# Optimization experiments

Hardware: AMD Instinct MI355X
Metric: run time of the kernel (lower is better)

Reference implementation:

```python
import jax, jax.numpy as jnp
import numpy as np

VOCAB, DIM, HEADS, LAYERS = 32000, 1024, 16, 2
B, S = 2, 1024
HD = DIM // HEADS


def rmsnorm(x, g, eps=1e-6):
    return x * jax.lax.rsqrt(jnp.mean(x * x, axis=-1, keepdims=True) + eps) * g


def setup_inputs() -> dict:
    key = jax.random.key(0)
    ks = jax.random.split(key, 20)
    s = 0.02
    d = {
        "text_ids": jax.random.randint(ks[0], (B, S), 0, VOCAB),
        "embed": jax.random.normal(ks[1], (VOCAB, DIM), jnp.float32) * s,
        "g1": jnp.ones((LAYERS, DIM), jnp.float32),
        "wq": jax.random.normal(ks[2], (LAYERS, DIM, DIM), jnp.float32) * s,
        "bq": jnp.zeros((LAYERS, DIM), jnp.float32),
        "wk": jax.random.normal(ks[3], (LAYERS, DIM, DIM), jnp.float32) * s,
        "bk": jnp.zeros((LAYERS, DIM), jnp.float32),
        "wv": jax.random.normal(ks[4], (LAYERS, DIM, DIM), jnp.float32) * s,
        "bv": jnp.zeros((LAYERS, DIM), jnp.float32),
        "wo": jax.random.normal(ks[5], (LAYERS, DIM, DIM), jnp.float32) * s,
        "bo": jnp.zeros((LAYERS, DIM), jnp.float32),
        "g2": jnp.ones((LAYERS, DIM), jnp.float32),
        "w1": jax.random.normal(ks[6], (LAYERS, DIM, 4 * DIM), jnp.float32) * s,
        "b1": jnp.zeros((LAYERS, 4 * DIM), jnp.float32),
        "w2": jax.random.normal(ks[7], (LAYERS, 4 * DIM, DIM), jnp.float32) * s,
        "b2": jnp.zeros((LAYERS, DIM), jnp.float32),
        "gf": jnp.ones((DIM,), jnp.float32),
        "head_w": jax.random.normal(ks[8], (DIM, VOCAB), jnp.float32) * s,
        "head_b": jnp.zeros((VOCAB,), jnp.float32),
    }
    return d


def reference(text_ids, embed, g1, wq, bq, wk, bk, wv, bv, wo, bo,
              g2, w1, b1, w2, b2, gf, head_w, head_b):
    b, s = text_ids.shape
    x = embed[text_ids]                                   # [B,S,D]
    causal = jnp.tril(jnp.ones((s, s), dtype=bool))        # [S,S]
    scale = 1.0 / jnp.sqrt(jnp.asarray(HD, x.dtype))
    for l in range(LAYERS):
        # attention sublayer: x = x + attn(norm1(x))
        h = rmsnorm(x, g1[l])
        q = (h @ wq[l] + bq[l]).reshape(b, s, HEADS, HD)
        k = (h @ wk[l] + bk[l]).reshape(b, s, HEADS, HD)
        v = (h @ wv[l] + bv[l]).reshape(b, s, HEADS, HD)
        scores = jnp.einsum("bqhd,bkhd->bhqk", q, k) * scale
        scores = jnp.where(causal, scores, jnp.asarray(-1e30, scores.dtype))
        a = jax.nn.softmax(scores, axis=-1)
        o = jnp.einsum("bhqk,bkhd->bqhd", a, v).reshape(b, s, DIM)
        x = x + (o @ wo[l] + bo[l])
        # FFN sublayer: x = x + ffn(norm2(x)), SiLU MLP (MoE unused in source forward)
        h2 = rmsnorm(x, g2[l])
        x = x + (jax.nn.silu(h2 @ w1[l] + b1[l]) @ w2[l] + b2[l])
    x = rmsnorm(x, gf)
    return x.astype(jnp.float32) @ head_w + head_b         # [B,S,VOCAB]
```

## Files before the change

kernel.cpp:

```cpp
#include <hip/hip_runtime.h>

#define LAYERS 2
#define DIM 1024
#define HEADS 16
#define HD 64
#define BATCH 2
#define SEQ 1024
#define ROWS (BATCH * SEQ)
#define FFN (4 * DIM)
#define VOCAB 32000
#define QKVN (3 * DIM)

typedef unsigned short u16;
typedef short vshort8 __attribute__((ext_vector_type(8)));
typedef float f32x4 __attribute__((ext_vector_type(4)));

#define VMCNT(n) asm volatile("s_waitcnt vmcnt(" #n ")" ::: "memory")

__device__ __forceinline__ u16 f2bf(float f) {
  union { float f; unsigned u; } x{f};
  unsigned r = (x.u + 0x7fffu + ((x.u >> 16) & 1u)) >> 16;
  return (u16)r;
}

__device__ __forceinline__ void gll16(const void* g, u16* l) {
  __builtin_amdgcn_global_load_lds(
      (const __attribute__((address_space(1))) void*)g,
      (__attribute__((address_space(3))) void*)l, 16, 0, 0);
}

__device__ __forceinline__ int xcd_swizzle(int orig, int nwg) {
  int q = nwg >> 3, r = nwg & 7;
  int xcd = orig & 7;
  int base = (xcd < r) ? xcd * (q + 1) : r * (q + 1) + (xcd - r) * q;
  return base + (orig >> 3);
}

__global__ __launch_bounds__(256) void transpose_f32_bf16(
    const float* __restrict__ src, u16* __restrict__ dst, int R, int C) {
  __shared__ float tile[32][33];
  int c0 = blockIdx.x * 32, r0 = blockIdx.y * 32;
  int tx = threadIdx.x, ty = threadIdx.y;
#pragma unroll
  for (int i = 0; i < 4; i++)
    tile[ty + i * 8][tx] = src[(size_t)(r0 + ty + i * 8) * C + c0 + tx];
  __syncthreads();
#pragma unroll
  for (int i = 0; i < 4; i++)
    dst[(size_t)(c0 + ty + i * 8) * R + r0 + tx] = f2bf(tile[tx][ty + i * 8]);
}

__global__ __launch_bounds__(256) void pack_qkv_bias(
    const float* __restrict__ bq, const float* __restrict__ bk,
    const float* __restrict__ bv, float* __restrict__ o) {
  int t = blockIdx.x * 256 + threadIdx.x;
  if (t < DIM) o[t] = bq[t];
  else if (t < 2 * DIM) o[t] = bk[t - DIM];
  else if (t < 3 * DIM) o[t] = bv[t - 2 * DIM];
}

__global__ __launch_bounds__(256) void embed_gather(
    const int* __restrict__ ids, const float* __restrict__ emb,
    float* __restrict__ x) {
  int row = blockIdx.x;
  int id = ids[row];
  const float4* s = (const float4*)(emb + (size_t)id * DIM);
  float4* d = (float4*)(x + (size_t)row * DIM);
  d[threadIdx.x] = s[threadIdx.x];
}

__global__ __launch_bounds__(256) void rmsnorm_kernel(
    const float* __restrict__ x, const float* __restrict__ g,
    u16* __restrict__ out) {
  int row = blockIdx.x;
  int t = threadIdx.x;
  const float4* xr = (const float4*)(x + (size_t)row * DIM);
  float4 v = xr[t];
  float ss = v.x * v.x + v.y * v.y + v.z * v.z + v.w * v.w;
  for (int off = 32; off > 0; off >>= 1) ss += __shfl_down(ss, off);
  __shared__ float part[4];
  if ((t & 63) == 0) part[t >> 6] = ss;
  __syncthreads();
  float tot = part[0] + part[1] + part[2] + part[3];
  float r = rsqrtf(tot / (float)DIM + 1e-6f);
  float4 gv = ((const float4*)g)[t];
  ushort4 o;
  o.x = f2bf(v.x * r * gv.x);
  o.y = f2bf(v.y * r * gv.y);
  o.z = f2bf(v.z * r * gv.z);
  o.w = f2bf(v.w * r * gv.w);
  *(ushort4*)(out + (size_t)row * DIM + t * 4) = o;
}

__global__ __launch_bounds__(256) void addnorm_kernel(
    float* __restrict__ x, const float* __restrict__ P0,
    const float* __restrict__ P1, const float* __restrict__ bias,
    const float* __restrict__ g, u16* __restrict__ h) {
  int row = blockIdx.x;
  int t = threadIdx.x;
  float4 v = ((const float4*)(x + (size_t)row * DIM))[t];
  float4 a = ((const float4*)(P0 + (size_t)row * DIM))[t];
  float4 b = ((const float4*)(P1 + (size_t)row * DIM))[t];
  float4 c = ((const float4*)bias)[t];
  v.x += a.x + b.x + c.x;
  v.y += a.y + b.y + c.y;
  v.z += a.z + b.z + c.z;
  v.w += a.w + b.w + c.w;
  ((float4*)(x + (size_t)row * DIM))[t] = v;
  float ss = v.x * v.x + v.y * v.y + v.z * v.z + v.w * v.w;
  for (int off = 32; off > 0; off >>= 1) ss += __shfl_down(ss, off);
  __shared__ float part[4];
  if ((t & 63) == 0) part[t >> 6] = ss;
  __syncthreads();
  float tot = part[0] + part[1] + part[2] + part[3];
  float r = rsqrtf(tot / (float)DIM + 1e-6f);
  float4 gv = ((const float4*)g)[t];
  ushort4 o;
  o.x = f2bf(v.x * r * gv.x);
  o.y = f2bf(v.y * r * gv.y);
  o.z = f2bf(v.z * r * gv.z);
  o.w = f2bf(v.w * r * gv.w);
  *(ushort4*)(h + (size_t)row * DIM + t * 4) = o;
}

template <int OUTBF, int SILU, int SPLITK, int MFAST>
__global__ __launch_bounds__(256, 2) void gemm128_kernel(
    const u16* __restrict__ A, const u16* __restrict__ Wt,
    const float* __restrict__ bias, void* __restrict__ outv,
    float* __restrict__ pout1, int M, int N, int K) {
  __shared__ u16 As[2][128 * 64];
  __shared__ u16 Bs[2][128 * 64];
  int nm = M >> 7, nn = N >> 7, nwg = nm * nn;
  int wg = xcd_swizzle(blockIdx.x, SPLITK ? nwg * 2 : nwg);
  int ks = 0;
  if (SPLITK) { ks = wg >= nwg; wg -= ks * nwg; }
  int mi, ni;
  if (MFAST) { mi = wg % nm; ni = wg / nm; }
  else       { ni = wg % nn; mi = wg / nn; }
  int m0 = mi << 7, n0 = ni << 7;
  int kb = SPLITK ? ks * (K >> 1) : 0;
  int NTt = (SPLITK ? (K >> 1) : K) >> 6;
  int tid = threadIdx.x, wave = tid >> 6, lane = tid & 63;
  int wr = wave >> 1, wc = wave & 1;
  int r16 = lane & 15, g4 = lane >> 4;
  int lrow = lane >> 3, lslot = lane & 7;

  f32x4 acc[4][4] = {};

  auto stage = [&](int buf, int kt) {
#pragma unroll
    for (int i = 0; i < 4; i++) {
      int s = wave * 4 + i;
      int row = s * 8 + lrow;
      int slot = lslot ^ (row & 7);
      gll16(A + (size_t)(m0 + row) * K + kb + kt * 64 + slot * 8,
            &As[buf][s * 512 + lane * 8]);
    }
#pragma unroll
    for (int i = 0; i < 4; i++) {
      int s = wave * 4 + i;
      int row = s * 8 + lrow;
      int slot = lslot ^ (row & 7);
      gll16(Wt + (size_t)(n0 + row) * K + kb + kt * 64 + slot * 8,
            &Bs[buf][s * 512 + lane * 8]);
    }
  };

  stage(0, 0);
  VMCNT(0);
  __builtin_amdgcn_s_barrier();

  for (int t = 0; t < NTt; t++) {
    int cur = t & 1;
    if (t + 1 < NTt) stage(cur ^ 1, t + 1);
#pragma unroll
    for (int kk = 0; kk < 2; kk++) {
      vshort8 af[4], bf[4];
#pragma unroll
      for (int m = 0; m < 4; m++) {
        int r = wr * 64 + m * 16 + r16;
        int slot = (kk * 4 + g4) ^ (r & 7);
        af[m] = *(const vshort8*)&As[cur][r * 64 + slot * 8];
      }
#pragma unroll
      for (int n = 0; n < 4; n++) {
        int c = wc * 64 + n * 16 + r16;
        int slot = (kk * 4 + g4) ^ (c & 7);
        bf[n] = *(const vshort8*)&Bs[cur][c * 64 + slot * 8];
      }
#pragma unroll
      for (int m = 0; m < 4; m++)
#pragma unroll
        for (int n = 0; n < 4; n++)
          acc[m][n] = __builtin_amdgcn_mfma_f32_16x16x32_bf16(af[m], bf[n],
                                                              acc[m][n], 0, 0, 0);
    }
    VMCNT(0);
    __builtin_amdgcn_s_barrier();
  }

  if (SPLITK) {
    float* P = ks ? pout1 : (float*)outv;
#pragma unroll
    for (int m = 0; m < 4; m++) {
      int rowb = m0 + wr * 64 + m * 16 + g4 * 4;
#pragma unroll
      for (int n = 0; n < 4; n++) {
        int col = n0 + wc * 64 + n * 16 + r16;
#pragma unroll
        for (int j = 0; j < 4; j++)
          P[(size_t)(rowb + j) * N + col] = acc[m][n][j];
      }
    }
  } else {
#pragma unroll
    for (int m = 0; m < 4; m++) {
      int rowb = m0 + wr * 64 + m * 16 + g4 * 4;
#pragma unroll
      for (int n = 0; n < 4; n++) {
        int col = n0 + wc * 64 + n * 16 + r16;
        float b = bias[col];
#pragma unroll
        for (int j = 0; j < 4; j++) {
          float v = acc[m][n][j] + b;
          if (SILU) v = v / (1.f + __expf(-v));
          if (OUTBF)
            ((u16*)outv)[(size_t)(rowb + j) * N + col] = f2bf(v);
          else
            ((float*)outv)[(size_t)(rowb + j) * N + col] = v;
        }
      }
    }
  }
}

__global__ __launch_bounds__(512, 2) void gemm256_kernel(
    const u16* __restrict__ A, const u16* __restrict__ Wt,
    const float* __restrict__ bias, float* __restrict__ out,
    int M, int N, int K) {
  __shared__ u16 As[2][256 * 64];
  __shared__ u16 Bs[2][256 * 64];
  int nm = M >> 8, nn = N >> 8;
  int wg = xcd_swizzle(blockIdx.x, nm * nn);
  int mi = wg % nm, ni = wg / nm;
  int m0 = mi << 8, n0 = ni << 8;
  int tid = threadIdx.x, w = tid >> 6, lane = tid & 63;
  int wr = w >> 2, wc = w & 3;
  int r16 = lane & 15, g4 = lane >> 4;
  int srow8 = lane >> 3, sslot = lane & 7;
  int NT = K >> 6;

  f32x4 acc[8][4] = {};

  auto stageA = [&](int buf, int t, int hb, int j) {
    int chunk = j * 8 + w;
    int row = hb * 128 + chunk * 8 + srow8;
    int slot = sslot ^ (row & 7);
    gll16(A + (size_t)(m0 + row) * K + t * 64 + slot * 8,
          &As[buf][hb * 8192 + chunk * 512 + lane * 8]);
  };
  auto stageB = [&](int buf, int t, int hb, int j) {
    int chunk = j * 8 + w;
    int row = hb * 128 + chunk * 8 + srow8;
    int slot = sslot ^ (row & 7);
    gll16(Wt + (size_t)(n0 + row) * K + t * 64 + slot * 8,
          &Bs[buf][hb * 8192 + chunk * 512 + lane * 8]);
  };
  auto readA = [&](int buf, int mf, int kk) -> vshort8 {
    int row = mf * 32 + wr * 16 + r16;
    int slot = (kk * 4 + g4) ^ (row & 7);
    return *(const vshort8*)&As[buf][row * 64 + slot * 8];
  };
  auto readB = [&](int buf, int nf, int kk) -> vshort8 {
    int row = nf * 64 + wc * 16 + r16;
    int slot = (kk * 4 + g4) ^ (row & 7);
    return *(const vshort8*)&Bs[buf][row * 64 + slot * 8];
  };

  stageA(0, 0, 0, 0); stageA(0, 0, 0, 1);
  stageB(0, 0, 0, 0); stageB(0, 0, 0, 1);
  stageB(0, 0, 1, 0); stageB(0, 0, 1, 1);
  stageA(0, 0, 1, 0); stageA(0, 0, 1, 1);
  VMCNT(0);
  __builtin_amdgcn_s_barrier();

  vshort8 af[4][2], bf0[2][2], bf1[2][2];

  for (int t = 0; t < NT; t++) {
    int cur = t & 1, nxt = cur ^ 1;
    bool hn = (t + 1 < NT);
#pragma unroll
    for (int m = 0; m < 4; m++)
#pragma unroll
      for (int kk = 0; kk < 2; kk++) af[m][kk] = readA(cur, m, kk);
#pragma unroll
    for (int n = 0; n < 2; n++)
#pragma unroll
      for (int kk = 0; kk < 2; kk++) bf0[n][kk] = readB(cur, n, kk);
    if (hn) { stageA(nxt, t + 1, 0, 0); stageA(nxt, t + 1, 0, 1); }
    __builtin_amdgcn_s_barrier();
    __builtin_amdgcn_s_setprio(1);
#pragma unroll
    for (int m = 0; m < 4; m++)
#pragma unroll
      for (int n = 0; n < 2; n++)
#pragma unroll
        for (int kk = 0; kk < 2; kk++)
          acc[m][n] = __builtin_amdgcn_mfma_f32_16x16x32_bf16(
              af[m][kk], bf0[n][kk], acc[m][n], 0, 0, 0);
    __builtin_amdgcn_s_setprio(0);
    VMCNT(4);
    __builtin_amdgcn_s_barrier();
#pragma unroll
    for (int n = 0; n < 2; n++)
#pragma unroll
      for (int kk = 0; kk < 2; kk++) bf1[n][kk] = readB(cur, 2 + n, kk);
    if (hn) { stageB(nxt, t + 1, 0, 0); stageB(nxt, t + 1, 0, 1); }
    __builtin_amdgcn_s_barrier();
    __builtin_amdgcn_s_setprio(1);
#pragma unroll
    for (int m = 0; m < 4; m++)
#pragma unroll
      for (int n = 0; n < 2; n++)
#pragma unroll
        for (int kk = 0; kk < 2; kk++)
          acc[m][n + 2] = __builtin_amdgcn_mfma_f32_16x16x32_bf16(
              af[m][kk], bf1[n][kk], acc[m][n + 2], 0, 0, 0);
    __builtin_amdgcn_s_setprio(0);
    VMCNT(4);
    __builtin_amdgcn_s_barrier();
#pragma unroll
    for (int m = 0; m < 4; m++)
#pragma unroll
      for (int kk = 0; kk < 2; kk++) af[m][kk] = readA(cur, 4 + m, kk);
    if (hn) { stageB(nxt, t + 1, 1, 0); stageB(nxt, t + 1, 1, 1); }
    __builtin_amdgcn_s_barrier();
    __builtin_amdgcn_s_setprio(1);
#pragma unroll
    for (int m = 0; m < 4; m++)
#pragma unroll
      for (int n = 0; n < 2; n++)
#pragma unroll
        for (int kk = 0; kk < 2; kk++)
          acc[m + 4][n + 2] = __builtin_amdgcn_mfma_f32_16x16x32_bf16(
              af[m][kk], bf1[n][kk], acc[m + 4][n + 2], 0, 0, 0);
    __builtin_amdgcn_s_setprio(0);
    VMCNT(4);
    __builtin_amdgcn_s_barrier();
#pragma unroll
    for (int n = 0; n < 2; n++)
#pragma unroll
      for (int kk = 0; kk < 2; kk++) bf0[n][kk] = readB(cur, n, kk);
    if (hn) { stageA(nxt, t + 1, 1, 0); stageA(nxt, t + 1, 1, 1); }
    __builtin_amdgcn_s_barrier();
    __builtin_amdgcn_s_setprio(1);
#pragma unroll
    for (int m = 0; m < 4; m++)
#pragma unroll
      for (int n = 0; n < 2; n++)
#pragma unroll
        for (int kk = 0; kk < 2; kk++)
          acc[m + 4][n] = __builtin_amdgcn_mfma_f32_16x16x32_bf16(
              af[m][kk], bf0[n][kk], acc[m + 4][n], 0, 0, 0);
    __builtin_amdgcn_s_setprio(0);
    VMCNT(4);
    __builtin_amdgcn_s_barrier();
  }

#pragma unroll
  for (int mf = 0; mf < 8; mf++) {
    int rowb = m0 + mf * 32 + wr * 16 + g4 * 4;
#pragma unroll
    for (int nf = 0; nf < 4; nf++) {
      int col = n0 + nf * 64 + wc * 16 + r16;
      float b = bias[col];
#pragma unroll
      for (int j = 0; j < 4; j++)
        out[(size_t)(rowb + j) * N + col] = acc[mf][nf][j] + b;
    }
  }
}

__global__ __launch_bounds__(256) void vtrans_kernel(const u16* __restrict__ qkv,
                                                     u16* __restrict__ vt2) {
  __shared__ u16 tl[64][80];
  int s0 = blockIdx.x * 64;
  int bh = blockIdx.y;
  int b = bh >> 4, h = bh & 15;
  int tid = threadIdx.x;
#pragma unroll
  for (int c = 0; c < 2; c++) {
    int idx = tid + c * 256;
    int row = idx >> 3;
    int col8 = (idx & 7) * 8;
    *(vshort8*)&tl[row][col8] = *(const vshort8*)
        &qkv[(size_t)(b * SEQ + s0 + row) * QKVN + 2 * DIM + h * HD + col8];
  }
  __syncthreads();
#pragma unroll
  for (int c = 0; c < 2; c++) {
    int idx = tid + c * 256;
    int s8l = idx >> 6;
    int d = idx & 63;
    vshort8 v;
#pragma unroll
    for (int j = 0; j < 8; j++) v[j] = (short)tl[s8l * 8 + j][d];
    *(vshort8*)&vt2[(((size_t)bh * (SEQ / 8) + (s0 >> 3) + s8l) * 64 + d) * 8] = v;
  }
}

__global__ __launch_bounds__(256) void attn_kernel(const u16* __restrict__ qkv,
                                                   const u16* __restrict__ vt2,
                                                   u16* __restrict__ o) {
  __shared__ u16 Ks[2][32 * 64];
  __shared__ u16 pl[4][16 * 40];
  int qblk = blockIdx.x, bh = blockIdx.y;
  int b = bh >> 4, h = bh & 15;
  int tid = threadIdx.x, w = tid >> 6, lane = tid & 63;
  int r16 = lane & 15, g4 = lane >> 4;
  int q0 = qblk * 64 + w * 16;

  const u16* qrow = qkv + ((size_t)(b * SEQ) + q0 + r16) * QKVN + h * HD;
  vshort8 aq0 = *(const vshort8*)(qrow + g4 * 8);
  vshort8 aq1 = *(const vshort8*)(qrow + 32 + g4 * 8);

  float mrun[4], lrun[4];
  f32x4 accO[4];
#pragma unroll
  for (int j = 0; j < 4; j++) { mrun[j] = -1e30f; lrun[j] = 0.f; }
#pragma unroll
  for (int d = 0; d < 4; d++) accO[d] = f32x4{0.f, 0.f, 0.f, 0.f};

  int nkvT = qblk * 2 + 2;
  auto stageK = [&](int buf, int kt) {
    int row = tid >> 3;
    int slot = (tid & 7) ^ (row & 7);
    gll16(qkv + ((size_t)(b * SEQ) + kt * 32 + row) * QKVN + DIM + h * HD + slot * 8,
          &Ks[buf][w * 512 + lane * 8]);
  };
  stageK(0, 0);
  __syncthreads();
  int buf = 0;
  for (int kt = 0; kt < nkvT; kt++) {
    int kv0 = kt * 32;
    if (kt + 1 < nkvT) stageK(buf ^ 1, kt + 1);
    if (kv0 <= q0 + 15) {
      int row0 = r16, row1 = 16 + r16;
      vshort8 bk00 = *(const vshort8*)&Ks[buf][row0 * 64 + ((0 + g4) ^ (row0 & 7)) * 8];
      vshort8 bk01 = *(const vshort8*)&Ks[buf][row0 * 64 + ((4 + g4) ^ (row0 & 7)) * 8];
      vshort8 bk10 = *(const vshort8*)&Ks[buf][row1 * 64 + ((0 + g4) ^ (row1 & 7)) * 8];
      vshort8 bk11 = *(const vshort8*)&Ks[buf][row1 * 64 + ((4 + g4) ^ (row1 & 7)) * 8];
      f32x4 s0 = {}, s1 = {};
      s0 = __builtin_amdgcn_mfma_f32_16x16x32_bf16(aq0, bk00, s0, 0, 0, 0);
      s0 = __builtin_amdgcn_mfma_f32_16x16x32_bf16(aq1, bk01, s0, 0, 0, 0);
      s1 = __builtin_amdgcn_mfma_f32_16x16x32_bf16(aq0, bk10, s1, 0, 0, 0);
      s1 = __builtin_amdgcn_mfma_f32_16x16x32_bf16(aq1, bk11, s1, 0, 0, 0);

#pragma unroll
      for (int j = 0; j < 4; j++) {
        int qg = q0 + g4 * 4 + j;
        float x0 = s0[j] * 0.125f;
        float x1 = s1[j] * 0.125f;
        if (kv0 + r16 > qg) x0 = -1e30f;
        if (kv0 + 16 + r16 > qg) x1 = -1e30f;
        float mx = fmaxf(x0, x1);
#pragma unroll
        for (int mm = 1; mm < 16; mm <<= 1) mx = fmaxf(mx, __shfl_xor(mx, mm));
        float mnew = fmaxf(mrun[j], mx);
        float alpha = __expf(mrun[j] - mnew);
        float p0 = __expf(x0 - mnew);
        float p1 = __expf(x1 - mnew);
        float rs = p0 + p1;
#pragma unroll
        for (int mm = 1; mm < 16; mm <<= 1) rs += __shfl_xor(rs, mm);
        lrun[j] = lrun[j] * alpha + rs;
        mrun[j] = mnew;
#pragma unroll
        for (int d = 0; d < 4; d++) accO[d][j] *= alpha;
        pl[w][(g4 * 4 + j) * 40 + r16] = f2bf(p0);
        pl[w][(g4 * 4 + j) * 40 + 16 + r16] = f2bf(p1);
      }
      asm volatile("s_waitcnt lgkmcnt(0)" ::: "memory");
      vshort8 ap = *(const vshort8*)&pl[w][r16 * 40 + g4 * 8];
      const u16* vbase = vt2 + (((size_t)bh * (SEQ / 8) + (kv0 >> 3) + g4) * 64) * 8;
#pragma unroll
      for (int d = 0; d < 4; d++) {
        vshort8 bv = *(const vshort8*)(vbase + (size_t)(d * 16 + r16) * 8);
        accO[d] = __builtin_amdgcn_mfma_f32_16x16x32_bf16(ap, bv, accO[d], 0, 0, 0);
      }
    }
    __syncthreads();
    buf ^= 1;
  }

#pragma unroll
  for (int j = 0; j < 4; j++) {
    float inv = 1.f / lrun[j];
    int row = q0 + g4 * 4 + j;
#pragma unroll
    for (int d = 0; d < 4; d++)
      o[((size_t)(b * SEQ) + row) * DIM + h * HD + d * 16 + r16] =
          f2bf(accO[d][j] * inv);
  }
}

extern "C" void kernel_launch(void* const* d_in, const int* in_sizes, int n_in,
                              void* d_out, int out_size, void* d_ws,
                              size_t ws_size, hipStream_t stream) {
  const int* ids = (const int*)d_in[0];
  const float* emb = (const float*)d_in[1];
  const float* g1 = (const float*)d_in[2];
  const float* wq = (const float*)d_in[3];
  const float* bq = (const float*)d_in[4];
  const float* wk = (const float*)d_in[5];
  const float* bk = (const float*)d_in[6];
  const float* wv = (const float*)d_in[7];
  const float* bv = (const float*)d_in[8];
  const float* wo = (const float*)d_in[9];
  const float* bo = (const float*)d_in[10];
  const float* g2 = (const float*)d_in[11];
  const float* w1 = (const float*)d_in[12];
  const float* b1 = (const float*)d_in[13];
  const float* w2 = (const float*)d_in[14];
  const float* b2 = (const float*)d_in[15];
  const float* gf = (const float*)d_in[16];
  const float* head_w = (const float*)d_in[17];
  const float* head_b = (const float*)d_in[18];
  float* out = (float*)d_out;

  char* ws = (char*)d_ws;
  size_t off = 0;
  auto alloc = [&](size_t bytes) -> char* {
    char* p = ws + off;
    off += (bytes + 255) & ~(size_t)255;
    return p;
  };
  u16* wqkvT = (u16*)alloc((size_t)LAYERS * QKVN * DIM * 2);
  u16* woT = (u16*)alloc((size_t)LAYERS * DIM * DIM * 2);
  u16* w1T = (u16*)alloc((size_t)LAYERS * DIM * FFN * 2);
  u16* w2T = (u16*)alloc((size_t)LAYERS * DIM * FFN * 2);
  u16* headT = (u16*)alloc((size_t)VOCAB * DIM * 2);
  float* bqkv = (float*)alloc((size_t)LAYERS * QKVN * 4);
  float* x = (float*)alloc((size_t)ROWS * DIM * 4);
  u16* h = (u16*)alloc((size_t)ROWS * DIM * 2);
  u16* qkvb = (u16*)alloc((size_t)ROWS * QKVN * 2);
  u16* vtb = (u16*)alloc((size_t)ROWS * DIM * 2);
  u16* ob = (u16*)alloc((size_t)ROWS * DIM * 2);
  u16* tb = (u16*)alloc((size_t)ROWS * FFN * 2);
  float* P0 = (float*)alloc((size_t)ROWS * DIM * 4);
  float* P1 = (float*)alloc((size_t)ROWS * DIM * 4);
  if (off > ws_size) return;

  dim3 tb32(32, 8);
  for (int l = 0; l < LAYERS; l++) {
    u16* base = wqkvT + (size_t)l * QKVN * DIM;
    transpose_f32_bf16<<<dim3(DIM / 32, DIM / 32), tb32, 0, stream>>>(
        wq + (size_t)l * DIM * DIM, base, DIM, DIM);
    transpose_f32_bf16<<<dim3(DIM / 32, DIM / 32), tb32, 0, stream>>>(
        wk + (size_t)l * DIM * DIM, base + (size_t)DIM * DIM, DIM, DIM);
    transpose_f32_bf16<<<dim3(DIM / 32, DIM / 32), tb32, 0, stream>>>(
        wv + (size_t)l * DIM * DIM, base + (size_t)2 * DIM * DIM, DIM, DIM);
    transpose_f32_bf16<<<dim3(DIM / 32, DIM / 32), tb32, 0, stream>>>(
        wo + (size_t)l * DIM * DIM, woT + (size_t)l * DIM * DIM, DIM, DIM);
    transpose_f32_bf16<<<dim3(FFN / 32, DIM / 32), tb32, 0, stream>>>(
        w1 + (size_t)l * DIM * FFN, w1T + (size_t)l * DIM * FFN, DIM, FFN);
    transpose_f32_bf16<<<dim3(DIM / 32, FFN / 32), tb32, 0, stream>>>(
        w2 + (size_t)l * DIM * FFN, w2T + (size_t)l * DIM * FFN, FFN, DIM);
    pack_qkv_bias<<<QKVN / 256, 256, 0, stream>>>(
        bq + (size_t)l * DIM, bk + (size_t)l * DIM, bv + (size_t)l * DIM,
        bqkv + (size_t)l * QKVN);
  }
  transpose_f32_bf16<<<dim3(VOCAB / 32, DIM / 32), tb32, 0, stream>>>(
      head_w, headT, DIM, VOCAB);

  embed_gather<<<ROWS, 256, 0, stream>>>(ids, emb, x);
  rmsnorm_kernel<<<ROWS, 256, 0, stream>>>(x, g1, h);

  for (int l = 0; l < LAYERS; l++) {
    gemm128_kernel<1, 0, 0, 1>
        <<<(ROWS / 128) * (QKVN / 128), 256, 0, stream>>>(
            h, wqkvT + (size_t)l * QKVN * DIM, bqkv + (size_t)l * QKVN,
            qkvb, nullptr, ROWS, QKVN, DIM);
    vtrans_kernel<<<dim3(SEQ / 64, BATCH * HEADS), 256, 0, stream>>>(qkvb, vtb);
    attn_kernel<<<dim3(SEQ / 64, BATCH * HEADS), 256, 0, stream>>>(qkvb, vtb, ob);
    gemm128_kernel<0, 0, 1, 0>
        <<<2 * (ROWS / 128) * (DIM / 128), 256, 0, stream>>>(
            ob, woT + (size_t)l * DIM * DIM, nullptr, P0, P1, ROWS, DIM, DIM);
    addnorm_kernel<<<ROWS, 256, 0, stream>>>(
        x, P0, P1, bo + (size_t)l * DIM, g2 + (size_t)l * DIM, h);
    gemm128_kernel<1, 1, 0, 1>
        <<<(ROWS / 128) * (FFN / 128), 256, 0, stream>>>(
            h, w1T + (size_t)l * DIM * FFN, b1 + (size_t)l * FFN, tb, nullptr,
            ROWS, FFN, DIM);
    gemm128_kernel<0, 0, 1, 0>
        <<<2 * (ROWS / 128) * (DIM / 128), 256, 0, stream>>>(
            tb, w2T + (size_t)l * DIM * FFN, nullptr, P0, P1, ROWS, DIM, FFN);
    addnorm_kernel<<<ROWS, 256, 0, stream>>>(
        x, P0, P1, b2 + (size_t)l * DIM,
        (l == LAYERS - 1) ? gf : (g1 + (size_t)(l + 1) * DIM), h);
  }
  gemm256_kernel<<<(ROWS / 256) * (VOCAB / 256), 512, 0, stream>>>(
      h, headT, head_b, out, ROWS, VOCAB, DIM);
}
```

Before: 670.9 us.

## Make vocab head GEMM persistent over M tiles with cross-tile prefetch

Replaces the head GEMM's one-tile-per-block grid with 250 blocks. Each block owns one 256-column vocab strip and walks four consecutive 256-row M tiles, with the K-loop double-buffer prefetch running on into the next M tile. The aim is to remove the wave-quantization tail, overlap the tile-boundary prologue, and keep the weight strip warm in cache. It also drops a redundant LDS reload of B fragments that were already held in registers. The cost is only about one block per CU instead of two, which reduces latency hiding, and the epilogue stores now sit inside the persistent loop and can stall the pipeline.

After: 634.2 us. 1.06x faster.

```diff
diff --git a/kernel.cpp b/kernel.cpp
--- a/kernel.cpp
+++ b/kernel.cpp
@@ -234,36 +234,37 @@
   }
 }
 
-__global__ __launch_bounds__(512, 2) void gemm256_kernel(
+__global__ __launch_bounds__(512, 2) void gemm256p_kernel(
     const u16* __restrict__ A, const u16* __restrict__ Wt,
     const float* __restrict__ bias, float* __restrict__ out,
     int M, int N, int K) {
   __shared__ u16 As[2][256 * 64];
   __shared__ u16 Bs[2][256 * 64];
-  int nm = M >> 8, nn = N >> 8;
-  int wg = xcd_swizzle(blockIdx.x, nm * nn);
-  int mi = wg % nm, ni = wg / nm;
-  int m0 = mi << 8, n0 = ni << 8;
+  int nn = N >> 8;
+  int wg = xcd_swizzle(blockIdx.x, nn * 2);
+  int ni = wg >> 1, mhalf = wg & 1;
+  int n0 = ni << 8;
   int tid = threadIdx.x, w = tid >> 6, lane = tid & 63;
   int wr = w >> 2, wc = w & 3;
   int r16 = lane & 15, g4 = lane >> 4;
   int srow8 = lane >> 3, sslot = lane & 7;
-  int NT = K >> 6;
+  const int NTK = 16;
+  const int NGT = 64;
 
   f32x4 acc[8][4] = {};
 
-  auto stageA = [&](int buf, int t, int hb, int j) {
+  auto stageA = [&](int buf, int mb, int kt, int hb, int j) {
     int chunk = j * 8 + w;
     int row = hb * 128 + chunk * 8 + srow8;
     int slot = sslot ^ (row & 7);
-    gll16(A + (size_t)(m0 + row) * K + t * 64 + slot * 8,
+    gll16(A + (size_t)(mb + row) * K + kt * 64 + slot * 8,
           &As[buf][hb * 8192 + chunk * 512 + lane * 8]);
   };
-  auto stageB = [&](int buf, int t, int hb, int j) {
+  auto stageB = [&](int buf, int kt, int hb, int j) {
     int chunk = j * 8 + w;
     int row = hb * 128 + chunk * 8 + srow8;
     int slot = sslot ^ (row & 7);
-    gll16(Wt + (size_t)(n0 + row) * K + t * 64 + slot * 8,
+    gll16(Wt + (size_t)(n0 + row) * K + kt * 64 + slot * 8,
           &Bs[buf][hb * 8192 + chunk * 512 + lane * 8]);
   };
   auto readA = [&](int buf, int mf, int kk) -> vshort8 {
@@ -277,107 +278,114 @@
     return *(const vshort8*)&Bs[buf][row * 64 + slot * 8];
   };
 
-  stageA(0, 0, 0, 0); stageA(0, 0, 0, 1);
-  stageB(0, 0, 0, 0); stageB(0, 0, 0, 1);
-  stageB(0, 0, 1, 0); stageB(0, 0, 1, 1);
-  stageA(0, 0, 1, 0); stageA(0, 0, 1, 1);
+  int mb0 = (mhalf * 4) << 8;
+  stageA(0, mb0, 0, 0, 0); stageA(0, mb0, 0, 0, 1);
+  stageB(0, 0, 0, 0);      stageB(0, 0, 0, 1);
+  stageB(0, 0, 1, 0);      stageB(0, 0, 1, 1);
+  stageA(0, mb0, 0, 1, 0); stageA(0, mb0, 0, 1, 1);
   VMCNT(0);
   __builtin_amdgcn_s_barrier();
 
   vshort8 af[4][2], bf0[2][2], bf1[2][2];
 
-  for (int t = 0; t < NT; t++) {
-    int cur = t & 1, nxt = cur ^ 1;
-    bool hn = (t + 1 < NT);
-#pragma unroll
-    for (int m = 0; m < 4; m++)
-#pragma unroll
-      for (int kk = 0; kk < 2; kk++) af[m][kk] = readA(cur, m, kk);
-#pragma unroll
-    for (int n = 0; n < 2; n++)
-#pragma unroll
-      for (int kk = 0; kk < 2; kk++) bf0[n][kk] = readB(cur, n, kk);
-    if (hn) { stageA(nxt, t + 1, 0, 0); stageA(nxt, t + 1, 0, 1); }
-    __builtin_amdgcn_s_barrier();
-    __builtin_amdgcn_s_setprio(1);
-#pragma unroll
-    for (int m = 0; m < 4; m++)
+  for (int ti = 0; ti < 4; ti++) {
+    int m0 = (mhalf * 4 + ti) << 8;
+    for (int tt = 0; tt < NTK; tt++) {
+      int gt = ti * NTK + tt;
+      int cur = gt & 1, nxt = cur ^ 1;
+      int gt1 = gt + 1;
+      bool hn = gt1 < NGT;
+      int kt1 = gt1 & (NTK - 1);
+      int mb1 = (mhalf * 4 + (gt1 >> 4)) << 8;
+#pragma unroll
+      for (int m = 0; m < 4; m++)
+#pragma unroll
+        for (int kk = 0; kk < 2; kk++) af[m][kk] = readA(cur, m, kk);
 #pragma unroll
       for (int n = 0; n < 2; n++)
 #pragma unroll
-        for (int kk = 0; kk < 2; kk++)
-          acc[m][n] = __builtin_amdgcn_mfma_f32_16x16x32_bf16(
-              af[m][kk], bf0[n][kk], acc[m][n], 0, 0, 0);
-    __builtin_amdgcn_s_setprio(0);
-    VMCNT(4);
-    __builtin_amdgcn_s_barrier();
-#pragma unroll
-    for (int n = 0; n < 2; n++)
-#pragma unroll
-      for (int kk = 0; kk < 2; kk++) bf1[n][kk] = readB(cur, 2 + n, kk);
-    if (hn) { stageB(nxt, t + 1, 0, 0); stageB(nxt, t + 1, 0, 1); }
-    __builtin_amdgcn_s_barrier();
-    __builtin_amdgcn_s_setprio(1);
-#pragma unroll
-    for (int m = 0; m < 4; m++)
+        for (int kk = 0; kk < 2; kk++) bf0[n][kk] = readB(cur, n, kk);
+      if (hn) { stageA(nxt, mb1, kt1, 0, 0); stageA(nxt, mb1, kt1, 0, 1); }
+      __builtin_amdgcn_s_barrier();
+      __builtin_amdgcn_s_setprio(1);
+#pragma unroll
+      for (int m = 0; m < 4; m++)
+#pragma unroll
+        for (int n = 0; n < 2; n++)
+#pragma unroll
+          for (int kk = 0; kk < 2; kk++)
+            acc[m][n] = __builtin_amdgcn_mfma_f32_16x16x32_bf16(
+                af[m][kk], bf0[n][kk], acc[m][n], 0, 0, 0);
+      __builtin_amdgcn_s_setprio(0);
+      VMCNT(4);
+      __builtin_amdgcn_s_barrier();
 #pragma unroll
       for (int n = 0; n < 2; n++)
 #pragma unroll
-        for (int kk = 0; kk < 2; kk++)
-          acc[m][n + 2] = __builtin_amdgcn_mfma_f32_16x16x32_bf16(
-              af[m][kk], bf1[n][kk], acc[m][n + 2], 0, 0, 0);
-    __builtin_amdgcn_s_setprio(0);
-    VMCNT(4);
-    __builtin_amdgcn_s_barrier();
-#pragma unroll
-    for (int m = 0; m < 4; m++)
-#pragma unroll
-      for (int kk = 0; kk < 2; kk++) af[m][kk] = readA(cur, 4 + m, kk);
-    if (hn) { stageB(nxt, t + 1, 1, 0); stageB(nxt, t + 1, 1, 1); }
-    __builtin_amdgcn_s_barrier();
-    __builtin_amdgcn_s_setprio(1);
-#pragma unroll
-    for (int m = 0; m < 4; m++)
-#pragma unroll
-      for (int n = 0; n < 2; n++)
-#pragma unroll
-        for (int kk = 0; kk < 2; kk++)
-          acc[m + 4][n + 2] = __builtin_amdgcn_mfma_f32_16x16x32_bf16(
-              af[m][kk], bf1[n][kk], acc[m + 4][n + 2], 0, 0, 0);
-    __builtin_amdgcn_s_setprio(0);
-    VMCNT(4);
-    __builtin_amdgcn_s_barrier();
-#pragma unroll
-    for (int n = 0; n < 2; n++)
-#pragma unroll
-      for (int kk = 0; kk < 2; kk++) bf0[n][kk] = readB(cur, n, kk);
-    if (hn) { stageA(nxt, t + 1, 1, 0); stageA(nxt, t + 1, 1, 1); }
-    __builtin_amdgcn_s_barrier();
-    __builtin_amdgcn_s_setprio(1);
-#pragma unroll
-    for (int m = 0; m < 4; m++)
-#pragma unroll
-      for (int n = 0; n < 2; n++)
-#pragma unroll
-        for (int kk = 0; kk < 2; kk++)
-          acc[m + 4][n] = __builtin_amdgcn_mfma_f32_16x16x32_bf16(
-              af[m][kk], bf0[n][kk], acc[m + 4][n], 0, 0, 0);
-    __builtin_amdgcn_s_setprio(0);
-    VMCNT(4);
-    __builtin_amdgcn_s_barrier();
-  }
-
-#pragma unroll
-  for (int mf = 0; mf < 8; mf++) {
-    int rowb = m0 + mf * 32 + wr * 16 + g4 * 4;
-#pragma unroll
-    for (int nf = 0; nf < 4; nf++) {
-      int col = n0 + nf * 64 + wc * 16 + r16;
-      float b = bias[col];
-#pragma unroll
-      for (int j = 0; j < 4; j++)
-        out[(size_t)(rowb + j) * N + col] = acc[mf][nf][j] + b;
-    }
+        for (int kk = 0; kk < 2; kk++) bf1[n][kk] = readB(cur, 2 + n, kk);
+      if (hn) { stageB(nxt, kt1, 0, 0); stageB(nxt, kt1, 0, 1); }
+      __builtin_amdgcn_s_barrier();
+      __builtin_amdgcn_s_setprio(1);
+#pragma unroll
+      for (int m = 0; m < 4; m++)
+#pragma unroll
+        for (int n = 0; n < 2; n++)
+#pragma unroll
+          for (int kk = 0; kk < 2; kk++)
+            acc[m][n + 2] = __builtin_amdgcn_mfma_f32_16x16x32_bf16(
+                af[m][kk], bf1[n][kk], acc[m][n + 2], 0, 0, 0);
+      __builtin_amdgcn_s_setprio(0);
+      VMCNT(4);
+      __builtin_amdgcn_s_barrier();
+#pragma unroll
+      for (int m = 0; m < 4; m++)
+#pragma unroll
+        for (int kk = 0; kk < 2; kk++) af[m][kk] = readA(cur, 4 + m, kk);
+      if (hn) { stageB(nxt, kt1, 1, 0); stageB(nxt, kt1, 1, 1); }
+      __builtin_amdgcn_s_barrier();
+      __builtin_amdgcn_s_setprio(1);
+#pragma unroll
+      for (int m = 0; m < 4; m++)
+#pragma unroll
+        for (int n = 0; n < 2; n++)
+#pragma unroll
+          for (int kk = 0; kk < 2; kk++)
+            acc[m + 4][n + 2] = __builtin_amdgcn_mfma_f32_16x16x32_bf16(
+                af[m][kk], bf1[n][kk], acc[m + 4][n + 2], 0, 0, 0);
+      __builtin_amdgcn_s_setprio(0);
+      VMCNT(4);
+      __builtin_amdgcn_s_barrier();
+      if (hn) { stageA(nxt, mb1, kt1, 1, 0); stageA(nxt, mb1, kt1, 1, 1); }
+      __builtin_amdgcn_s_barrier();
+      __builtin_amdgcn_s_setprio(1);
+#pragma unroll
+      for (int m = 0; m < 4; m++)
+#pragma unroll
+        for (int n = 0; n < 2; n++)
+#pragma unroll
+          for (int kk = 0; kk < 2; kk++)
+            acc[m + 4][n] = __builtin_amdgcn_mfma_f32_16x16x32_bf16(
+                af[m][kk], bf0[n][kk], acc[m + 4][n], 0, 0, 0);
+      __builtin_amdgcn_s_setprio(0);
+      VMCNT(4);
+      __builtin_amdgcn_s_barrier();
+    }
+#pragma unroll
+    for (int mf = 0; mf < 8; mf++) {
+      int rowb = m0 + mf * 32 + wr * 16 + g4 * 4;
+#pragma unroll
+      for (int nf = 0; nf < 4; nf++) {
+        int col = n0 + nf * 64 + wc * 16 + r16;
+        float b = bias[col];
+#pragma unroll
+        for (int j = 0; j < 4; j++)
+          out[(size_t)(rowb + j) * N + col] = acc[mf][nf][j] + b;
+      }
+    }
+#pragma unroll
+    for (int mf = 0; mf < 8; mf++)
+#pragma unroll
+      for (int nf = 0; nf < 4; nf++) acc[mf][nf] = f32x4{0.f, 0.f, 0.f, 0.f};
   }
 }
 
@@ -599,6 +607,6 @@
         x, P0, P1, b2 + (size_t)l * DIM,
         (l == LAYERS - 1) ? gf : (g1 + (size_t)(l + 1) * DIM), h);
   }
-  gemm256_kernel<<<(ROWS / 256) * (VOCAB / 256), 512, 0, stream>>>(
+  gemm256p_kernel<<<(VOCAB / 256) * 2, 512, 0, stream>>>(
       h, headT, head_b, out, ROWS, VOCAB, DIM);
 }
```
